# Performance work log

Measured on AMD Instinct MI355X. Metric: run time of the kernel, lower is better.

The kernel has to match this reference:

```python
import jax, jax.numpy as jnp
import numpy as np

N_MBED = 384
HEAD_SIZE = 64

def setup_inputs() -> dict:
    key = jax.random.key(0)
    kx, kq, kk, kv = jax.random.split(key, 4)
    B, T = 128, 256
    x = jax.random.normal(kx, (B, T, N_MBED), dtype=jnp.float32)
    # torch nn.Linear(n_mbed, head_size, bias=False): y = x @ W^T, W:[head_size, n_mbed].
    # We store the transposed weight [n_mbed, head_size] so y = x @ W.
    s = 1.0 / np.sqrt(N_MBED)
    Wq = jax.random.uniform(kq, (N_MBED, HEAD_SIZE), jnp.float32, -s, s)
    Wk = jax.random.uniform(kk, (N_MBED, HEAD_SIZE), jnp.float32, -s, s)
    Wv = jax.random.uniform(kv, (N_MBED, HEAD_SIZE), jnp.float32, -s, s)
    return {"x": x, "Wq": Wq, "Wk": Wk, "Wv": Wv}

def reference(x, Wq, Wk, Wv):
    B, T, C = x.shape  # C = n_mbed = 384
    q = x @ Wq  # [B,T,H]
    k = x @ Wk
    v = x @ Wv
    # Faithful to source: wei = k @ q^T, scaled by C**-0.5 (C = n_mbed, not head_size)
    wei = jnp.einsum('bth,bsh->bts', k, q) * (C ** -0.5)  # [B,T,T]
    mask = jnp.tril(jnp.ones((T, T), dtype=bool))
    wei = jnp.where(mask, wei, -jnp.inf)
    wei = jax.nn.softmax(wei, axis=-1)
    # dropout omitted (eval mode / identity)
    out = jnp.einsum('bts,bsh->bth', wei, v)  # [B,T,H]
    return out
```

## Files before the change

kernel.cpp:

```cpp
#include <hip/hip_runtime.h>
#include <hip/hip_bf16.h>
#include <math.h>

constexpr int kB = 128;
constexpr int kT = 256;
constexpr int kC = 384;
constexpr int kH = 64;

using bf16x8 = __attribute__((ext_vector_type(8))) short;
using f32x4  = __attribute__((ext_vector_type(4))) float;

union BF8 { bf16x8 v; __hip_bfloat162 h[4]; };
union BF4 { short4 s; __hip_bfloat162 h[2]; };

__device__ inline bf16x8 cvt8(float4 a, float4 b) {
    BF8 u;
    u.h[0] = __float22bfloat162_rn(float2{a.x, a.y});
    u.h[1] = __float22bfloat162_rn(float2{a.z, a.w});
    u.h[2] = __float22bfloat162_rn(float2{b.x, b.y});
    u.h[3] = __float22bfloat162_rn(float2{b.z, b.w});
    return u.v;
}
__device__ inline short4 cvt4(float4 a) {
    BF4 u;
    u.h[0] = __float22bfloat162_rn(float2{a.x, a.y});
    u.h[1] = __float22bfloat162_rn(float2{a.z, a.w});
    return u.s;
}
__device__ inline short bf1(float f) {
    __hip_bfloat16 h = __float2bfloat16(f);
    return *(short*)&h;
}

__global__ void prep_kernel(const float* __restrict__ Wq,
                            const float* __restrict__ Wk,
                            const float* __restrict__ Wv,
                            __hip_bfloat16* __restrict__ Wt) {
    int idx = blockIdx.x * 256 + threadIdx.x;
    int n = idx / kC, c = idx % kC;
    int w = n >> 6, h = n & 63;
    const float* W = (w == 0) ? Wq : (w == 1) ? Wk : Wv;
    float val = W[c * kH + h];
    if (w == 1) val *= 0.051031036307982884f;
    Wt[idx] = __float2bfloat16(val);
}

__global__ __launch_bounds__(512, 2) void fused_kernel(
    const float* __restrict__ x, const __hip_bfloat16* __restrict__ Wt,
    float* __restrict__ out)
{
    __shared__ short Qs[256 * 68];
    __shared__ short VTs[64 * 260];
    __shared__ short Ks[128 * 68];
    __shared__ __attribute__((aligned(16))) char STG[73728];
    short (*As)[64 * 72]  = (short (*)[64 * 72])STG;
    short (*Bs)[192 * 72] = (short (*)[192 * 72])(STG + 18432);

    const int b    = blockIdx.y;
    const int half = (int)blockIdx.x ^ 1;
    const int t0   = half * 128;
    const int nmc  = (t0 + 128) >> 6;

    const int tid  = threadIdx.x;
    const int wave = tid >> 6, lane = tid & 63;
    const int m16  = lane & 15, quad = lane >> 4;
    const int wm = wave & 1, wn = wave >> 1;
    const short* wt = (const short*)Wt;
    const float* xb = x + (size_t)b * kT * kC;

    const bool stageA = (tid < 256);
    const int am  = tid >> 2;
    const int ak0 = (tid & 3) * 16;
    const int bu  = tid - 256;

    float4 la[4]; bf16x8 lb[6];
    auto glod = [&](int m0, int k0) {
        if (stageA) {
#pragma unroll
            for (int i = 0; i < 4; ++i)
                la[i] = *(const float4*)(xb + (size_t)(m0 + am) * kC + k0 + ak0 + 4 * i);
        } else {
#pragma unroll
            for (int i = 0; i < 6; ++i) {
                int c = bu + 256 * i;
                int n = c >> 3, kk = (c & 7) * 8;
                lb[i] = *(const bf16x8*)(wt + (size_t)n * kC + k0 + kk);
            }
        }
    };
    auto swr = [&](int d) {
        if (stageA) {
#pragma unroll
            for (int i = 0; i < 4; ++i)
                *(short4*)&As[d][am * 72 + ak0 + 4 * i] = cvt4(la[i]);
        } else {
#pragma unroll
            for (int i = 0; i < 6; ++i) {
                int c = bu + 256 * i;
                int n = c >> 3, kk = (c & 7) * 8;
                *(bf16x8*)&Bs[d][n * 72 + kk] = lb[i];
            }
        }
    };

    for (int mc = 0; mc < nmc; ++mc) {
        const int m0 = mc * 64;

        f32x4 acc[2][3];
#pragma unroll
        for (int mt = 0; mt < 2; ++mt)
#pragma unroll
            for (int j = 0; j < 3; ++j) acc[mt][j] = f32x4{0.f, 0.f, 0.f, 0.f};

        glod(m0, 0);
        swr(0);
        __syncthreads();

        for (int s = 0; s < 6; ++s) {
            const int d = s & 1;
            if (s < 5) glod(m0, (s + 1) * 64);
#pragma unroll
            for (int kf = 0; kf < 2; ++kf) {
                bf16x8 af[2], bfr[3];
#pragma unroll
                for (int mt = 0; mt < 2; ++mt)
                    af[mt] = *(const bf16x8*)&As[d][(wm * 32 + mt * 16 + m16) * 72 + kf * 32 + quad * 8];
#pragma unroll
                for (int j = 0; j < 3; ++j)
                    bfr[j] = *(const bf16x8*)&Bs[d][(wn * 48 + j * 16 + m16) * 72 + kf * 32 + quad * 8];
#pragma unroll
                for (int mt = 0; mt < 2; ++mt)
#pragma unroll
                    for (int j = 0; j < 3; ++j)
                        acc[mt][j] = __builtin_amdgcn_mfma_f32_16x16x32_bf16(
                            af[mt], bfr[j], acc[mt][j], 0, 0, 0);
            }
            if (s < 5) swr(d ^ 1);
            __syncthreads();
        }

#pragma unroll
        for (int mt = 0; mt < 2; ++mt) {
            const int mbase = m0 + wm * 32 + mt * 16 + quad * 4;
#pragma unroll
            for (int j = 0; j < 3; ++j) {
                const int n = wn * 48 + j * 16 + m16;
                const int w = n >> 6, h = n & 63;
                if (w == 2) {
                    float4 f = make_float4(acc[mt][j][0], acc[mt][j][1],
                                           acc[mt][j][2], acc[mt][j][3]);
                    *(short4*)&VTs[h * 260 + mbase] = cvt4(f);
                } else if (w == 1) {
                    if (m0 >= t0) {
#pragma unroll
                        for (int r = 0; r < 4; ++r)
                            Ks[(mbase + r - t0) * 68 + h] = bf1(acc[mt][j][r]);
                    }
                } else {
#pragma unroll
                    for (int r = 0; r < 4; ++r)
                        Qs[(mbase + r) * 68 + h] = bf1(acc[mt][j][r]);
                }
            }
        }
    }
    __syncthreads();

    const int wband = t0 + wave * 16;
    float* Pw = (float*)STG + wave * 16 * 68;

    const bf16x8 ka0 = *(const bf16x8*)&Ks[(wave * 16 + m16) * 68 + quad * 8];
    const bf16x8 ka1 = *(const bf16x8*)&Ks[(wave * 16 + m16) * 68 + quad * 8 + 32];

    f32x4 O[4];
    float m_[4], l_[4];
#pragma unroll
    for (int i = 0; i < 4; ++i) {
        O[i] = f32x4{0.f, 0.f, 0.f, 0.f};
        m_[i] = -INFINITY; l_[i] = 0.f;
    }

    const int ilast = wband >> 6;
    for (int i = 0; i <= ilast; ++i) {
        const bool diag = (i == ilast);
        const int jmax = diag ? (wave & 3) : 3;

        f32x4 S[4];
        const f32x4 Z = f32x4{0.f, 0.f, 0.f, 0.f};
#pragma unroll
        for (int j = 0; j < 4; ++j) {
            if (j <= jmax) {
                bf16x8 qb0 = *(const bf16x8*)&Qs[(i * 64 + j * 16 + m16) * 68 + quad * 8];
                bf16x8 qb1 = *(const bf16x8*)&Qs[(i * 64 + j * 16 + m16) * 68 + quad * 8 + 32];
                S[j] = __builtin_amdgcn_mfma_f32_16x16x32_bf16(ka0, qb0, Z, 0, 0, 0);
                S[j] = __builtin_amdgcn_mfma_f32_16x16x32_bf16(ka1, qb1, S[j], 0, 0, 0);
            }
        }
        if (diag) {
#pragma unroll
            for (int r = 0; r < 4; ++r)
                if (m16 > quad * 4 + r) S[jmax][r] = -INFINITY;
        }

        float P[4][4];
#pragma unroll
        for (int j = 0; j < 4; ++j)
#pragma unroll
            for (int r = 0; r < 4; ++r) P[j][r] = 0.f;
#pragma unroll
        for (int r = 0; r < 4; ++r) {
            float rm = -INFINITY;
#pragma unroll
            for (int j = 0; j < 4; ++j)
                if (j <= jmax) rm = fmaxf(rm, S[j][r]);
            rm = fmaxf(rm, __shfl_xor(rm, 1, 64));
            rm = fmaxf(rm, __shfl_xor(rm, 2, 64));
            rm = fmaxf(rm, __shfl_xor(rm, 4, 64));
            rm = fmaxf(rm, __shfl_xor(rm, 8, 64));
            const float mn = fmaxf(m_[r], rm);
            const float al = __expf(m_[r] - mn);
            m_[r] = mn;
            float rs = 0.f;
#pragma unroll
            for (int j = 0; j < 4; ++j) {
                if (j <= jmax) { P[j][r] = __expf(S[j][r] - mn); rs += P[j][r]; }
            }
            rs += __shfl_xor(rs, 1, 64);
            rs += __shfl_xor(rs, 2, 64);
            rs += __shfl_xor(rs, 4, 64);
            rs += __shfl_xor(rs, 8, 64);
            l_[r] = l_[r] * al + rs;
            O[0][r] *= al; O[1][r] *= al; O[2][r] *= al; O[3][r] *= al;
        }

#pragma unroll
        for (int j = 0; j < 4; ++j)
#pragma unroll
            for (int r = 0; r < 4; ++r)
                Pw[(quad * 4 + r) * 68 + j * 16 + m16] = P[j][r];
        const float* pr = Pw + m16 * 68 + quad * 8;
        bf16x8 pf0 = cvt8(*(const float4*)pr,        *(const float4*)(pr + 4));
        bf16x8 pf1 = cvt8(*(const float4*)(pr + 32), *(const float4*)(pr + 36));

#pragma unroll
        for (int ht = 0; ht < 4; ++ht) {
            bf16x8 vb0 = *(const bf16x8*)&VTs[(ht * 16 + m16) * 260 + i * 64 + quad * 8];
            bf16x8 vb1 = *(const bf16x8*)&VTs[(ht * 16 + m16) * 260 + i * 64 + quad * 8 + 32];
            O[ht] = __builtin_amdgcn_mfma_f32_16x16x32_bf16(pf0, vb0, O[ht], 0, 0, 0);
            O[ht] = __builtin_amdgcn_mfma_f32_16x16x32_bf16(pf1, vb1, O[ht], 0, 0, 0);
        }
    }

#pragma unroll
    for (int r = 0; r < 4; ++r) {
        const float inv = 1.f / l_[r];
        const size_t row = (size_t)(b * kT + wband + quad * 4 + r);
#pragma unroll
        for (int ht = 0; ht < 4; ++ht)
            out[row * kH + ht * 16 + m16] = O[ht][r] * inv;
    }
}

extern "C" void kernel_launch(void* const* d_in, const int* in_sizes, int n_in,
                              void* d_out, int out_size, void* d_ws, size_t ws_size,
                              hipStream_t stream) {
    const float* x  = (const float*)d_in[0];
    const float* Wq = (const float*)d_in[1];
    const float* Wk = (const float*)d_in[2];
    const float* Wv = (const float*)d_in[3];
    float* out = (float*)d_out;

    __hip_bfloat16* Wt = (__hip_bfloat16*)d_ws;

    prep_kernel<<<(192 * kC) / 256, 256, 0, stream>>>(Wq, Wk, Wv, Wt);
    fused_kernel<<<dim3(2, kB), 512, 0, stream>>>(x, Wt, out);
}
```

Baseline: 123.5 us.

## Project all 256 rows in one pass with K-step 32 and larger wave tiles

Replaces the chunked QKV projection (64-row chunks, K-step 64, repeated per chunk) with a single pass over all 256 sequence rows. It uses K-steps of 32, and each wave holds an 8x3 grid of MFMA accumulators. The aim is to remove the per-chunk prologue, its barriers and pipeline refills, and to reuse each B fragment across more rows. In exchange, the first-half block now also projects rows it never uses. Accumulator register pressure also rises sharply under the 512-thread launch bound, which risks spills. LDS strides are changed to 72/264/40-short rows, and the P staging buffer is moved into the A staging area.

Measured after the change: 118.5 us. -4.0%, faster.

```diff
diff --git a/kernel.cpp b/kernel.cpp
--- a/kernel.cpp
+++ b/kernel.cpp
@@ -49,17 +49,15 @@
     const float* __restrict__ x, const __hip_bfloat16* __restrict__ Wt,
     float* __restrict__ out)
 {
-    __shared__ short Qs[256 * 68];
-    __shared__ short VTs[64 * 260];
-    __shared__ short Ks[128 * 68];
-    __shared__ __attribute__((aligned(16))) char STG[73728];
-    short (*As)[64 * 72]  = (short (*)[64 * 72])STG;
-    short (*Bs)[192 * 72] = (short (*)[192 * 72])(STG + 18432);
+    __shared__ short Qs[256 * 72];
+    __shared__ short Ks[128 * 72];
+    __shared__ short VTs[64 * 264];
+    __shared__ short As[2][256 * 40];
+    __shared__ short Bs[2][192 * 40];
 
     const int b    = blockIdx.y;
     const int half = (int)blockIdx.x ^ 1;
     const int t0   = half * 128;
-    const int nmc  = (t0 + 128) >> 6;
 
     const int tid  = threadIdx.x;
     const int wave = tid >> 6, lane = tid & 63;
@@ -68,109 +66,102 @@
     const short* wt = (const short*)Wt;
     const float* xb = x + (size_t)b * kT * kC;
 
-    const bool stageA = (tid < 256);
-    const int am  = tid >> 2;
-    const int ak0 = (tid & 3) * 16;
-    const int bu  = tid - 256;
-
-    float4 la[4]; bf16x8 lb[6];
-    auto glod = [&](int m0, int k0) {
-        if (stageA) {
-#pragma unroll
-            for (int i = 0; i < 4; ++i)
-                la[i] = *(const float4*)(xb + (size_t)(m0 + am) * kC + k0 + ak0 + 4 * i);
-        } else {
-#pragma unroll
-            for (int i = 0; i < 6; ++i) {
-                int c = bu + 256 * i;
-                int n = c >> 3, kk = (c & 7) * 8;
-                lb[i] = *(const bf16x8*)(wt + (size_t)n * kC + k0 + kk);
-            }
+    const int arow = tid >> 1, acol = (tid & 1) * 16;
+
+    float4 la[4]; bf16x8 lb0, lb1;
+    auto glod = [&](int k0) {
+#pragma unroll
+        for (int i = 0; i < 4; ++i)
+            la[i] = *(const float4*)(xb + (size_t)arow * kC + k0 + acol + 4 * i);
+        {
+            int n = tid >> 2, kk = (tid & 3) * 8;
+            lb0 = *(const bf16x8*)(wt + (size_t)n * kC + k0 + kk);
+        }
+        if (tid < 256) {
+            int c = tid + 512;
+            int n = c >> 2, kk = (c & 3) * 8;
+            lb1 = *(const bf16x8*)(wt + (size_t)n * kC + k0 + kk);
         }
     };
     auto swr = [&](int d) {
-        if (stageA) {
-#pragma unroll
-            for (int i = 0; i < 4; ++i)
-                *(short4*)&As[d][am * 72 + ak0 + 4 * i] = cvt4(la[i]);
-        } else {
-#pragma unroll
-            for (int i = 0; i < 6; ++i) {
-                int c = bu + 256 * i;
-                int n = c >> 3, kk = (c & 7) * 8;
-                *(bf16x8*)&Bs[d][n * 72 + kk] = lb[i];
+#pragma unroll
+        for (int i = 0; i < 4; ++i)
+            *(short4*)&As[d][arow * 40 + acol + 4 * i] = cvt4(la[i]);
+        {
+            int n = tid >> 2, kk = (tid & 3) * 8;
+            *(bf16x8*)&Bs[d][n * 40 + kk] = lb0;
+        }
+        if (tid < 256) {
+            int c = tid + 512;
+            int n = c >> 2, kk = (c & 3) * 8;
+            *(bf16x8*)&Bs[d][n * 40 + kk] = lb1;
+        }
+    };
+
+    f32x4 acc[8][3];
+#pragma unroll
+    for (int mt = 0; mt < 8; ++mt)
+#pragma unroll
+        for (int j = 0; j < 3; ++j) acc[mt][j] = f32x4{0.f, 0.f, 0.f, 0.f};
+
+    glod(0);
+    swr(0);
+    __syncthreads();
+
+    for (int s = 0; s < 12; ++s) {
+        const int d = s & 1;
+        if (s < 11) glod((s + 1) * 32);
+
+        bf16x8 af[8], bfr[3];
+#pragma unroll
+        for (int j = 0; j < 3; ++j)
+            bfr[j] = *(const bf16x8*)&Bs[d][((wn * 3 + j) * 16 + m16) * 40 + quad * 8];
+#pragma unroll
+        for (int mt = 0; mt < 8; ++mt)
+            af[mt] = *(const bf16x8*)&As[d][(wm * 128 + mt * 16 + m16) * 40 + quad * 8];
+#pragma unroll
+        for (int mt = 0; mt < 8; ++mt)
+#pragma unroll
+            for (int j = 0; j < 3; ++j)
+                acc[mt][j] = __builtin_amdgcn_mfma_f32_16x16x32_bf16(
+                    af[mt], bfr[j], acc[mt][j], 0, 0, 0);
+
+        if (s < 11) swr(d ^ 1);
+        __syncthreads();
+    }
+
+#pragma unroll
+    for (int mt = 0; mt < 8; ++mt) {
+        const int mbase = wm * 128 + mt * 16 + quad * 4;
+#pragma unroll
+        for (int j = 0; j < 3; ++j) {
+            const int nt = wn * 3 + j;
+            const int w  = nt >> 2;
+            const int h  = (nt & 3) * 16 + m16;
+            if (w == 2) {
+                float4 f = make_float4(acc[mt][j][0], acc[mt][j][1],
+                                       acc[mt][j][2], acc[mt][j][3]);
+                *(short4*)&VTs[h * 264 + mbase] = cvt4(f);
+            } else if (w == 1) {
+                if ((mbase >> 7) == half) {
+#pragma unroll
+                    for (int r = 0; r < 4; ++r)
+                        Ks[(mbase + r - t0) * 72 + h] = bf1(acc[mt][j][r]);
+                }
+            } else {
+#pragma unroll
+                for (int r = 0; r < 4; ++r)
+                    Qs[(mbase + r) * 72 + h] = bf1(acc[mt][j][r]);
             }
         }
-    };
-
-    for (int mc = 0; mc < nmc; ++mc) {
-        const int m0 = mc * 64;
-
-        f32x4 acc[2][3];
-#pragma unroll
-        for (int mt = 0; mt < 2; ++mt)
-#pragma unroll
-            for (int j = 0; j < 3; ++j) acc[mt][j] = f32x4{0.f, 0.f, 0.f, 0.f};
-
-        glod(m0, 0);
-        swr(0);
-        __syncthreads();
-
-        for (int s = 0; s < 6; ++s) {
-            const int d = s & 1;
-            if (s < 5) glod(m0, (s + 1) * 64);
-#pragma unroll
-            for (int kf = 0; kf < 2; ++kf) {
-                bf16x8 af[2], bfr[3];
-#pragma unroll
-                for (int mt = 0; mt < 2; ++mt)
-                    af[mt] = *(const bf16x8*)&As[d][(wm * 32 + mt * 16 + m16) * 72 + kf * 32 + quad * 8];
-#pragma unroll
-                for (int j = 0; j < 3; ++j)
-                    bfr[j] = *(const bf16x8*)&Bs[d][(wn * 48 + j * 16 + m16) * 72 + kf * 32 + quad * 8];
-#pragma unroll
-                for (int mt = 0; mt < 2; ++mt)
-#pragma unroll
-                    for (int j = 0; j < 3; ++j)
-                        acc[mt][j] = __builtin_amdgcn_mfma_f32_16x16x32_bf16(
-                            af[mt], bfr[j], acc[mt][j], 0, 0, 0);
-            }
-            if (s < 5) swr(d ^ 1);
-            __syncthreads();
-        }
-
-#pragma unroll
-        for (int mt = 0; mt < 2; ++mt) {
-            const int mbase = m0 + wm * 32 + mt * 16 + quad * 4;
-#pragma unroll
-            for (int j = 0; j < 3; ++j) {
-                const int n = wn * 48 + j * 16 + m16;
-                const int w = n >> 6, h = n & 63;
-                if (w == 2) {
-                    float4 f = make_float4(acc[mt][j][0], acc[mt][j][1],
-                                           acc[mt][j][2], acc[mt][j][3]);
-                    *(short4*)&VTs[h * 260 + mbase] = cvt4(f);
-                } else if (w == 1) {
-                    if (m0 >= t0) {
-#pragma unroll
-                        for (int r = 0; r < 4; ++r)
-                            Ks[(mbase + r - t0) * 68 + h] = bf1(acc[mt][j][r]);
-                    }
-                } else {
-#pragma unroll
-                    for (int r = 0; r < 4; ++r)
-                        Qs[(mbase + r) * 68 + h] = bf1(acc[mt][j][r]);
-                }
-            }
-        }
     }
     __syncthreads();
 
     const int wband = t0 + wave * 16;
-    float* Pw = (float*)STG + wave * 16 * 68;
-
-    const bf16x8 ka0 = *(const bf16x8*)&Ks[(wave * 16 + m16) * 68 + quad * 8];
-    const bf16x8 ka1 = *(const bf16x8*)&Ks[(wave * 16 + m16) * 68 + quad * 8 + 32];
+    float* Pw = (float*)(&As[0][0]) + wave * 16 * 68;
+
+    const bf16x8 ka0 = *(const bf16x8*)&Ks[(wave * 16 + m16) * 72 + quad * 8];
+    const bf16x8 ka1 = *(const bf16x8*)&Ks[(wave * 16 + m16) * 72 + quad * 8 + 32];
 
     f32x4 O[4];
     float m_[4], l_[4];
@@ -190,8 +181,8 @@
 #pragma unroll
         for (int j = 0; j < 4; ++j) {
             if (j <= jmax) {
-                bf16x8 qb0 = *(const bf16x8*)&Qs[(i * 64 + j * 16 + m16) * 68 + quad * 8];
-                bf16x8 qb1 = *(const bf16x8*)&Qs[(i * 64 + j * 16 + m16) * 68 + quad * 8 + 32];
+                bf16x8 qb0 = *(const bf16x8*)&Qs[(i * 64 + j * 16 + m16) * 72 + quad * 8];
+                bf16x8 qb1 = *(const bf16x8*)&Qs[(i * 64 + j * 16 + m16) * 72 + quad * 8 + 32];
                 S[j] = __builtin_amdgcn_mfma_f32_16x16x32_bf16(ka0, qb0, Z, 0, 0, 0);
                 S[j] = __builtin_amdgcn_mfma_f32_16x16x32_bf16(ka1, qb1, S[j], 0, 0, 0);
             }
@@ -244,8 +235,8 @@
 
 #pragma unroll
         for (int ht = 0; ht < 4; ++ht) {
-            bf16x8 vb0 = *(const bf16x8*)&VTs[(ht * 16 + m16) * 260 + i * 64 + quad * 8];
-            bf16x8 vb1 = *(const bf16x8*)&VTs[(ht * 16 + m16) * 260 + i * 64 + quad * 8 + 32];
+            bf16x8 vb0 = *(const bf16x8*)&VTs[(ht * 16 + m16) * 264 + i * 64 + quad * 8];
+            bf16x8 vb1 = *(const bf16x8*)&VTs[(ht * 16 + m16) * 264 + i * 64 + quad * 8 + 32];
             O[ht] = __builtin_amdgcn_mfma_f32_16x16x32_bf16(pf0, vb0, O[ht], 0, 0, 0);
             O[ht] = __builtin_amdgcn_mfma_f32_16x16x32_bf16(pf1, vb1, O[ht], 0, 0, 0);
         }
```
